# Kernel tuning notes

Hardware: AMD Instinct MI355X
Metric: run time of the kernel (lower is better)

Reference implementation:

```python
import jax, jax.numpy as jnp
import numpy as np

B, H, W = 16, 128, 128
CIN, HID, OUT = 1, 64, 1
WS, NH = 8, 4  # window size, num heads
HD = HID // NH  # head dim = 16


def setup_inputs() -> dict:
    key = jax.random.key(0)
    ks = jax.random.split(key, 32)
    s = 0.05
    d = {"x": jax.random.normal(ks[0], (B, H, W, CIN), jnp.float32)}
    ins = [CIN, HID]
    for l in range(2):
        cin = ins[l]
        kb = 1 + 7 * l
        d[f"conv_w{l}"] = jax.random.normal(ks[kb], (4 * HID, cin + HID, 3, 3), jnp.float32) * s
        d[f"conv_b{l}"] = jnp.zeros((4 * HID,), jnp.float32)
        d[f"px_w{l}"] = jax.random.normal(ks[kb + 1], (HID, cin, 3, 3), jnp.float32) * s
        d[f"py_w{l}"] = jax.random.normal(ks[kb + 2], (HID, cin, 3, 3), jnp.float32) * s
        d[f"qkv_w{l}"] = jax.random.normal(ks[kb + 3], (3 * HID, HID), jnp.float32) * s
        d[f"proj_w{l}"] = jax.random.normal(ks[kb + 4], (HID, HID), jnp.float32) * s
        d[f"proj_b{l}"] = jnp.zeros((HID,), jnp.float32)
    d["out_w"] = jax.random.normal(ks[20], (OUT, HID, 1, 1), jnp.float32) * s
    d["out_b"] = jnp.zeros((OUT,), jnp.float32)
    return d


def _conv(x, w, pad, b=None):
    y = jax.lax.conv_general_dilated(
        x, w, (1, 1), [(pad, pad), (pad, pad)],
        dimension_numbers=("NCHW", "OIHW", "NCHW"))
    if b is not None:
        y = y + b[None, :, None, None]
    return y


def _win_attn(x, qkv_w, proj_w, proj_b):
    # x: [B, H, W, C], H and W are multiples of WS (pad branch is a no-op)
    Bx, Hx, Wx, C = x.shape
    nw_h, nw_w = Hx // WS, Wx // WS
    xw = x.reshape(Bx, nw_h, WS, nw_w, WS, C).transpose(0, 1, 3, 2, 4, 5)
    xw = xw.reshape(-1, WS * WS, C)  # [N, T, C], N = B*nw_h*nw_w, T = 64
    qkv = (xw @ qkv_w.T).reshape(-1, WS * WS, 3, NH, HD).transpose(2, 0, 3, 1, 4)
    q, k, v = qkv[0], qkv[1], qkv[2]  # [N, NH, T, HD]
    attn = jax.nn.softmax(jnp.einsum("nhqd,nhkd->nhqk", q, k) * (HD ** -0.5), axis=-1)
    o = jnp.einsum("nhqk,nhkd->nhqd", attn, v).transpose(0, 2, 1, 3).reshape(-1, WS * WS, C)
    o = o @ proj_w.T + proj_b
    o = o.reshape(Bx, nw_h, nw_w, WS, WS, C).transpose(0, 1, 3, 2, 4, 5)
    return o.reshape(Bx, Hx, Wx, C)


def _cell(x, h, c, cw, cb, pxw, pyw, qw, pw, pb):
    # x: [B, Cin, H, W]; h, c: [B, HID, H, W]
    cc = _conv(jnp.concatenate([x, h], axis=1), cw, 1, cb)
    ci, cf, co, cg = jnp.split(cc, 4, axis=1)
    px = _conv(x, pxw, 1)
    py = _conv(x, pyw, 1)
    i = jax.nn.sigmoid(ci + px)
    f = jax.nn.sigmoid(cf + px)
    o = jax.nn.sigmoid(co + py)
    g = jnp.tanh(cg + py)
    c2 = f * c + i * g
    h2 = o * jnp.tanh(c2)
    h2 = _win_attn(h2.transpose(0, 2, 3, 1), qw, pw, pb).transpose(0, 3, 1, 2)
    return h2, c2


def reference(x, conv_w0, conv_b0, px_w0, py_w0, qkv_w0, proj_w0, proj_b0,
              conv_w1, conv_b1, px_w1, py_w1, qkv_w1, proj_w1, proj_b1,
              out_w, out_b):
    # 4D input path: [B,H,W,C] -> NCHW frame, seq_len = 1
    xin = x.transpose(0, 3, 1, 2)
    z = jnp.zeros((B, HID, H, W), x.dtype)
    h0, _ = _cell(xin, z, z, conv_w0, conv_b0, px_w0, py_w0, qkv_w0, proj_w0, proj_b0)
    h1, _ = _cell(h0, z, z, conv_w1, conv_b1, px_w1, py_w1, qkv_w1, proj_w1, proj_b1)
    out = _conv(h1, out_w, 0, out_b)  # 1x1 output conv on last layer's (T=1) output
    return out.transpose(0, 2, 3, 1)  # [B, H, W, OUT]
```

## Files before the change

kernel.cpp:

```cpp
#include <hip/hip_runtime.h>


#define DEVFN __device__ __forceinline__

typedef __attribute__((ext_vector_type(8))) short short8;
typedef __attribute__((ext_vector_type(4))) float f32x4;

DEVFN float sigmoidf_(float z) { return 1.0f / (1.0f + __expf(-z)); }

DEVFN float tanhf_(float x) {
    float e = __expf(2.0f * x);
    return 1.0f - 2.0f / (e + 1.0f);
}

DEVFN unsigned short f2bf(float f) {
    unsigned int u = __builtin_bit_cast(unsigned int, f);
    u += 0x7fffu + ((u >> 16) & 1u);
    return (unsigned short)(u >> 16);
}

DEVFN unsigned pkbf(float a, float b) {
    return (unsigned)f2bf(a) | ((unsigned)f2bf(b) << 16);
}

__global__ __launch_bounds__(256) void repack_kernel(
    const float* __restrict__ cw0, const float* __restrict__ pxw0, const float* __restrict__ pyw0,
    const float* __restrict__ cw1, const float* __restrict__ pxw1, const float* __restrict__ pyw1,
    const float* __restrict__ qkvw0, const float* __restrict__ projw0,
    const float* __restrict__ qkvw1, const float* __restrict__ projw1,
    unsigned short* __restrict__ pwc, float* __restrict__ pw0,
    unsigned short* __restrict__ qb0, unsigned short* __restrict__ pjb0,
    unsigned short* __restrict__ qb1, unsigned short* __restrict__ pjb1)
{
    int idx = blockIdx.x * 256 + threadIdx.x;
    if (idx < 184320) {
        int j = idx & 7;
        int lane = (idx >> 3) & 63;
        int ng = (idx >> 9) & 3;
        int t = idx >> 11;
        int kk = t % 18, g = t / 18;
        int c = ng * 16 + (lane & 15);
        int kcol = kk * 32 + (lane >> 4) * 8 + j;
        int pos = kcol >> 6, cin = kcol & 63;
        float v;
        if (g == 0)      v = cw1[((c      ) * 128 + cin) * 9 + pos];
        else if (g == 1) v = cw1[((128 + c) * 128 + cin) * 9 + pos];
        else if (g == 2) v = cw1[((192 + c) * 128 + cin) * 9 + pos];
        else if (g == 3) v = pxw1[(c * 64 + cin) * 9 + pos];
        else             v = pyw1[(c * 64 + cin) * 9 + pos];
        pwc[idx] = f2bf(v);
    } else if (idx < 187200) {
        int i2 = idx - 184320;
        int g = i2 / (9 * 64);
        int rem = i2 - g * (9 * 64);
        int pos = rem >> 6, c = rem & 63;
        float v;
        if (g == 0)      v = cw0[(c      ) * 585 + pos];
        else if (g == 1) v = cw0[(128 + c) * 585 + pos];
        else if (g == 2) v = cw0[(192 + c) * 585 + pos];
        else if (g == 3) v = pxw0[c * 9 + pos];
        else             v = pyw0[c * 9 + pos];
        pw0[i2] = v;
    } else if (idx < 187200 + 12288) {
        int i = idx - 187200;           qb0[i] = f2bf(qkvw0[i]);
    } else if (idx < 187200 + 24576) {
        int i = idx - 187200 - 12288;   qb1[i] = f2bf(qkvw1[i]);
    } else if (idx < 187200 + 24576 + 4096) {
        int i = idx - 187200 - 24576;   pjb0[i] = f2bf(projw0[i]);
    } else if (idx < 187200 + 24576 + 8192) {
        int i = idx - 187200 - 28672;   pjb1[i] = f2bf(projw1[i]);
    }
}

__global__ __launch_bounds__(256) void gates1_kernel(
    const float* __restrict__ x, const float* __restrict__ pw,
    const float* __restrict__ cb, unsigned short* __restrict__ dst)
{
    const int idx = blockIdx.x * 256 + threadIdx.x;
    const int pix = idx >> 4, ch0 = (idx & 15) * 4;
    const int b = pix >> 14, y = (pix >> 7) & 127, xq = pix & 127;

    float a[9];
#pragma unroll
    for (int dy = 0; dy < 3; ++dy)
#pragma unroll
        for (int dx = 0; dx < 3; ++dx) {
            int gy = y + dy - 1, gx = xq + dx - 1;
            a[dy * 3 + dx] = ((unsigned)gy < 128u && (unsigned)gx < 128u)
                ? x[(b * 128 + gy) * 128 + gx] : 0.f;
        }

    float acc[5][4];
#pragma unroll
    for (int g = 0; g < 5; ++g)
#pragma unroll
        for (int u = 0; u < 4; ++u) acc[g][u] = 0.f;

#pragma unroll
    for (int pos = 0; pos < 9; ++pos) {
        const float av = a[pos];
#pragma unroll
        for (int g = 0; g < 5; ++g) {
            const float4 w4 = *(const float4*)(pw + (g * 9 + pos) * 64 + ch0);
            acc[g][0] = fmaf(av, w4.x, acc[g][0]);
            acc[g][1] = fmaf(av, w4.y, acc[g][1]);
            acc[g][2] = fmaf(av, w4.z, acc[g][2]);
            acc[g][3] = fmaf(av, w4.w, acc[g][3]);
        }
    }

    float hv[4];
#pragma unroll
    for (int u = 0; u < 4; ++u) {
        float ci = acc[0][u] + cb[ch0 + u];
        float co = acc[1][u] + cb[128 + ch0 + u];
        float cg = acc[2][u] + cb[192 + ch0 + u];
        float iv = sigmoidf_(ci + acc[3][u]);
        float ov = sigmoidf_(co + acc[4][u]);
        float gv = tanhf_(cg + acc[4][u]);
        hv[u] = ov * tanhf_(iv * gv);
    }
    uint2 o;
    o.x = pkbf(hv[0], hv[1]);
    o.y = pkbf(hv[2], hv[3]);
    *(uint2*)(dst + (size_t)pix * 64 + ch0) = o;
}

__global__ __launch_bounds__(256, 3) void gates64_kernel(
    const unsigned short* __restrict__ src, const unsigned short* __restrict__ wtc,
    const float* __restrict__ cb, unsigned short* __restrict__ dst)
{
    __shared__ unsigned short lds[3 * 66 * 64];
    char* const sbase = (char*)lds;

    const int tid = threadIdx.x;
    const int bid = blockIdx.x;
    const int xt = bid & 1, y = (bid >> 1) & 127, b = bid >> 8;
    const int x0 = xt * 64;

    for (int i4 = tid; i4 < 3 * 66 * 8; i4 += 256) {
        int r = i4 / (66 * 8);
        int rem = i4 - r * (66 * 8);
        int xx = rem >> 3, c8 = rem & 7;
        int gy = y + r - 1, gx = x0 + xx - 1;
        uint4 wv = make_uint4(0, 0, 0, 0);
        if ((unsigned)gy < 128u && (unsigned)gx < 128u)
            wv = *(const uint4*)(src + (((size_t)(b * 128 + gy) * 128 + gx) * 64 + c8 * 8));
        int addr = ((r * 66 + xx) * 128 + c8 * 16) ^ ((xx & 7) << 4);
        *(uint4*)(sbase + addr) = wv;
    }
    __syncthreads();

    const int lane = tid & 63;
    const int wv_ = tid >> 6;
    const int r0 = lane & 15;
    const int hi = lane >> 4;
    const int wch = wv_ * 16 + r0;

    const unsigned short* wbase = wtc + (size_t)(wv_ * 64 + lane) * 8;

    f32x4 acc[4][5];
#pragma unroll
    for (int mt = 0; mt < 4; ++mt)
#pragma unroll
        for (int g = 0; g < 5; ++g) acc[mt][g] = (f32x4){0.f, 0.f, 0.f, 0.f};

#pragma unroll
    for (int kk = 0; kk < 18; ++kk) {
        const int pos = kk >> 1, dy = pos / 3, dx = pos % 3, chalf = kk & 1;
        const int swz = (((r0 + dx) & 7) << 4);
        short8 bfr[5];
#pragma unroll
        for (int g = 0; g < 5; ++g)
            bfr[g] = *(const short8*)(wbase + (g * 18 + kk) * 2048);
        short8 afr[4];
#pragma unroll
        for (int mt = 0; mt < 4; ++mt) {
            const int row = dy * 66 + mt * 16 + r0 + dx;
            const int addr = (row * 128 + chalf * 64 + hi * 16) ^ swz;
            afr[mt] = *(const short8*)(sbase + addr);
        }
#pragma unroll
        for (int mt = 0; mt < 4; ++mt)
#pragma unroll
            for (int g = 0; g < 5; ++g)
                acc[mt][g] = __builtin_amdgcn_mfma_f32_16x16x32_bf16(
                    afr[mt], bfr[g], acc[mt][g], 0, 0, 0);
    }

    const float bci = cb[wch], bco = cb[128 + wch], bcg = cb[192 + wch];
    const int rowbase = (b * 128 + y) * 128 + x0;
#pragma unroll
    for (int mt = 0; mt < 4; ++mt) {
#pragma unroll
        for (int rg = 0; rg < 4; ++rg) {
            const int px_i = mt * 16 + hi * 4 + rg;
            float ci = acc[mt][0][rg] + bci;
            float co = acc[mt][1][rg] + bco;
            float cg = acc[mt][2][rg] + bcg;
            float pxv = acc[mt][3][rg];
            float pyv = acc[mt][4][rg];
            float iv = sigmoidf_(ci + pxv);
            float ov = sigmoidf_(co + pyv);
            float gv = tanhf_(cg + pyv);
            dst[(size_t)(rowbase + px_i) * 64 + wch] = f2bf(ov * tanhf_(iv * gv));
        }
    }
}

template <int FUSE>
__global__ __launch_bounds__(256, 3) void attn_kernel(
    const unsigned short* __restrict__ src,
    const unsigned short* __restrict__ qkvwb,
    const unsigned short* __restrict__ projwb,
    const float* __restrict__ projb,
    unsigned short* __restrict__ dst,
    const float* __restrict__ outw,
    const float* __restrict__ outb,
    float* __restrict__ out)
{
    __shared__ char sm[49152];
    char* const Xs = sm;
    char* const Xo = sm + 8192;
    char* const Qa = sm + 16384;
    char* const Ka = sm + 24576;
    char* const VT = sm + 32768;
    char* const Ps = sm + 40960;

    const int tid = threadIdx.x;
    const int lane = tid & 63;
    const int w = __builtin_amdgcn_readfirstlane(tid >> 6);
    const int lo = lane & 15, hi = lane >> 4;
    const int wid = blockIdx.x;
    const int b = wid >> 8, rem = wid & 255, wy = rem >> 4, wx = rem & 15;
    const int pixbase = (b * 128 + wy * 8) * 128 + wx * 8;

    {
        const int t = tid >> 2, c0 = (tid & 3) * 16;
        const int pix = pixbase + (t >> 3) * 128 + (t & 7);
        const uint4* sp = (const uint4*)(src + (size_t)pix * 64 + c0);
        uint4 w0 = sp[0], w1 = sp[1];
        const int a = t * 128 + c0 * 2, sz = (t & 7) << 4;
        *(uint4*)(Xs + (a ^ sz)) = w0;
        *(uint4*)(Xs + ((a + 16) ^ sz)) = w1;
    }
    __syncthreads();

    const int trow = w * 16 + lo;
    const int tswz = (lo & 7) << 4;

#pragma unroll
    for (int h = 0; h < 4; ++h) {
        f32x4 cq = {0.f, 0.f, 0.f, 0.f}, ck = cq, cv = cq;
#pragma unroll
        for (int ks = 0; ks < 2; ++ks) {
            const int koff = hi * 8 + ks * 32;
            short8 xb = *(const short8*)(Xs + ((trow * 128 + koff * 2) ^ tswz));
            short8 aq = *(const short8*)(qkvwb + (h * 16 + lo) * 64 + koff);
            short8 ak = *(const short8*)(qkvwb + (64 + h * 16 + lo) * 64 + koff);
            short8 bv = *(const short8*)(qkvwb + (128 + h * 16 + lo) * 64 + koff);
            cq = __builtin_amdgcn_mfma_f32_16x16x32_bf16(aq, xb, cq, 0, 0, 0);
            ck = __builtin_amdgcn_mfma_f32_16x16x32_bf16(ak, xb, ck, 0, 0, 0);
            cv = __builtin_amdgcn_mfma_f32_16x16x32_bf16(xb, bv, cv, 0, 0, 0);
        }
        uint2 qw, kw, vw;
        qw.x = pkbf(cq[0] * 0.125f, cq[1] * 0.125f);
        qw.y = pkbf(cq[2] * 0.125f, cq[3] * 0.125f);
        kw.x = pkbf(ck[0], ck[1]); kw.y = pkbf(ck[2], ck[3]);
        vw.x = pkbf(cv[0], cv[1]); vw.y = pkbf(cv[2], cv[3]);
        *(uint2*)(Qa + ((trow * 128 + (h * 16 + hi * 4) * 2) ^ tswz)) = qw;
        *(uint2*)(Ka + ((trow * 128 + (h * 16 + hi * 4) * 2) ^ tswz)) = kw;
        *(uint2*)(VT + (((h * 16 + lo) * 128 + (w * 16 + hi * 4) * 2) ^ ((lo & 7) << 4))) = vw;
    }
    __syncthreads();

#pragma unroll 1
    for (int h = 0; h < 4; ++h) {
        const int hb = h * 32;
        short8 bq = *(const short8*)(Qa + ((trow * 128 + hb + (hi & 1) * 16) ^ tswz));
        f32x4 st[4];
#pragma unroll
        for (int mt = 0; mt < 4; ++mt) {
            short8 ak2 = *(const short8*)(Ka + (((mt * 16 + lo) * 128 + hb + (hi & 1) * 16) ^ ((lo & 7) << 4)));
            f32x4 z = {0.f, 0.f, 0.f, 0.f};
            st[mt] = __builtin_amdgcn_mfma_f32_16x16x32_bf16(ak2, bq, z, 0, 0, 0);
        }
        float mx = -1e30f;
#pragma unroll
        for (int mt = 0; mt < 4; ++mt)
#pragma unroll
            for (int r = 0; r < 4; ++r) mx = fmaxf(mx, st[mt][r]);
        mx = fmaxf(mx, __shfl_xor(mx, 16));
        mx = fmaxf(mx, __shfl_xor(mx, 32));
        float pv[16];
        float sum = 0.f;
#pragma unroll
        for (int mt = 0; mt < 4; ++mt)
#pragma unroll
            for (int r = 0; r < 4; ++r) {
                float e = __expf(st[mt][r] - mx);
                pv[mt * 4 + r] = e;
                sum += e;
            }
        sum += __shfl_xor(sum, 16);
        sum += __shfl_xor(sum, 32);
        const float rs = 1.0f / sum;
#pragma unroll
        for (int mt = 0; mt < 4; ++mt) {
            uint2 pw_;
            pw_.x = pkbf(pv[mt * 4 + 0] * rs, pv[mt * 4 + 1] * rs);
            pw_.y = pkbf(pv[mt * 4 + 2] * rs, pv[mt * 4 + 3] * rs);
            *(uint2*)(Ps + ((trow * 128 + (mt * 16 + hi * 4) * 2) ^ tswz)) = pw_;
        }
        f32x4 ot = {0.f, 0.f, 0.f, 0.f};
#pragma unroll
        for (int ks = 0; ks < 2; ++ks) {
            const int ko = (hi * 8 + ks * 32) * 2;
            short8 av = *(const short8*)(VT + (((h * 16 + lo) * 128 + ko) ^ ((lo & 7) << 4)));
            short8 bp = *(const short8*)(Ps + ((trow * 128 + ko) ^ tswz));
            ot = __builtin_amdgcn_mfma_f32_16x16x32_bf16(av, bp, ot, 0, 0, 0);
        }
        uint2 ow_;
        ow_.x = pkbf(ot[0], ot[1]); ow_.y = pkbf(ot[2], ot[3]);
        *(uint2*)(Xo + ((trow * 128 + (h * 16 + hi * 4) * 2) ^ tswz)) = ow_;
    }
    __syncthreads();

    f32x4 cy[4];
#pragma unroll
    for (int mt = 0; mt < 4; ++mt) cy[mt] = (f32x4){0.f, 0.f, 0.f, 0.f};
#pragma unroll
    for (int ks = 0; ks < 2; ++ks) {
        const int koff = hi * 8 + ks * 32;
        short8 bw = *(const short8*)(projwb + (w * 16 + lo) * 64 + koff);
#pragma unroll
        for (int mt = 0; mt < 4; ++mt) {
            short8 ax = *(const short8*)(Xo + (((mt * 16 + lo) * 128 + koff * 2) ^ ((lo & 7) << 4)));
            cy[mt] = __builtin_amdgcn_mfma_f32_16x16x32_bf16(ax, bw, cy[mt], 0, 0, 0);
        }
    }
    const float pb = projb[w * 16 + lo];

    if constexpr (FUSE == 0) {
#pragma unroll
        for (int mt = 0; mt < 4; ++mt) {
#pragma unroll
            for (int r = 0; r < 4; ++r) {
                const int tok = mt * 16 + hi * 4 + r;
                const int pix = pixbase + (tok >> 3) * 128 + (tok & 7);
                dst[(size_t)pix * 64 + w * 16 + lo] = f2bf(cy[mt][r] + pb);
            }
        }
    } else {
        const float owv = outw[w * 16 + lo];
        float* red = (float*)VT;
#pragma unroll
        for (int mt = 0; mt < 4; ++mt) {
#pragma unroll
            for (int r = 0; r < 4; ++r) {
                float s = (cy[mt][r] + pb) * owv;
                s += __shfl_xor(s, 1);
                s += __shfl_xor(s, 2);
                s += __shfl_xor(s, 4);
                s += __shfl_xor(s, 8);
                if (lo == 0) red[(mt * 16 + hi * 4 + r) * 4 + w] = s;
            }
        }
        __syncthreads();
        if (tid < 64) {
            const int tok = tid;
            float4 rv = *(const float4*)(red + tok * 4);
            const int pix = pixbase + (tok >> 3) * 128 + (tok & 7);
            out[pix] = (rv.x + rv.y) + (rv.z + rv.w) + outb[0];
        }
    }
}

extern "C" void kernel_launch(void* const* d_in, const int* in_sizes, int n_in,
                              void* d_out, int out_size, void* d_ws, size_t ws_size,
                              hipStream_t stream)
{
    const float* x      = (const float*)d_in[0];
    const float* cw0    = (const float*)d_in[1];
    const float* cb0    = (const float*)d_in[2];
    const float* pxw0   = (const float*)d_in[3];
    const float* pyw0   = (const float*)d_in[4];
    const float* qkvw0  = (const float*)d_in[5];
    const float* projw0 = (const float*)d_in[6];
    const float* projb0 = (const float*)d_in[7];
    const float* cw1    = (const float*)d_in[8];
    const float* cb1    = (const float*)d_in[9];
    const float* pxw1   = (const float*)d_in[10];
    const float* pyw1   = (const float*)d_in[11];
    const float* qkvw1  = (const float*)d_in[12];
    const float* projw1 = (const float*)d_in[13];
    const float* projb1 = (const float*)d_in[14];
    const float* outw   = (const float*)d_in[15];
    const float* outb   = (const float*)d_in[16];

    const size_t BUF = (size_t)16 * 128 * 128 * 64 * sizeof(float);
    char* ws = (char*)d_ws;
    unsigned short* bufA = (unsigned short*)ws;
    unsigned short* bufB = (unsigned short*)(ws + BUF);
    char* wsx = ws + 2 * BUF;
    unsigned short* pwc  = (unsigned short*)(wsx);
    float* pw0           = (float*)(wsx + 369664);
    unsigned short* qb0  = (unsigned short*)(wsx + 381440);
    unsigned short* pjb0 = (unsigned short*)(wsx + 406016);
    unsigned short* qb1  = (unsigned short*)(wsx + 414208);
    unsigned short* pjb1 = (unsigned short*)(wsx + 438784);

    repack_kernel<<<860, 256, 0, stream>>>(
        cw0, pxw0, pyw0, cw1, pxw1, pyw1,
        qkvw0, projw0, qkvw1, projw1,
        pwc, pw0, qb0, pjb0, qb1, pjb1);

    gates1_kernel<<<16384, 256, 0, stream>>>(x, pw0, cb0, bufA);
    attn_kernel<0><<<4096, 256, 0, stream>>>(bufA, qb0, pjb0, projb0, bufB,
                                             nullptr, nullptr, nullptr);
    gates64_kernel<<<4096, 256, 0, stream>>>(bufB, pwc, cb1, bufA);
    attn_kernel<1><<<4096, 256, 0, stream>>>(bufA, qb1, pjb1, projb1, nullptr,
                                             outw, outb, (float*)d_out);
}
```

Measured before the change: 341.0 us.

## Stage gates1 weights/inputs in LDS, coalesce attn stores, shrink LDS

gates1 now processes one 64-pixel row segment per block. It stages the 5x9x64 weights and the 3x66 input halo in shared memory and loops over 16 channels per thread instead of reloading them from global memory per thread. The first attention kernel writes its projected output to LDS (aliasing the Xs/Ps region), then does coalesced 16-byte stores per pixel rather than scattered 2-byte stores. Attention LDS drops to 40KB to allow more resident blocks, and gates64 launch bounds drop from 3 to 2 waves-per-SIMD minimum. The risks are an extra barrier in attn and lower parallelism in gates1.

```diff
diff --git a/kernel.cpp b/kernel.cpp
--- a/kernel.cpp
+++ b/kernel.cpp
@@ -76,57 +76,72 @@
     const float* __restrict__ x, const float* __restrict__ pw,
     const float* __restrict__ cb, unsigned short* __restrict__ dst)
 {
-    const int idx = blockIdx.x * 256 + threadIdx.x;
-    const int pix = idx >> 4, ch0 = (idx & 15) * 4;
-    const int b = pix >> 14, y = (pix >> 7) & 127, xq = pix & 127;
-
+    __shared__ float wlds[5 * 9 * 64];
+    __shared__ float xp[3 * 66];
+
+    const int tid = threadIdx.x;
+    const int bid = blockIdx.x;
+    const int xt = bid & 1, y = (bid >> 1) & 127, b = bid >> 8;
+    const int x0 = xt * 64;
+
+    for (int i = tid; i < 5 * 9 * 64; i += 256) wlds[i] = pw[i];
+    if (tid < 198) {
+        int r = tid / 66, c = tid - r * 66;
+        int gy = y + r - 1, gx = x0 + c - 1;
+        xp[tid] = ((unsigned)gy < 128u && (unsigned)gx < 128u)
+            ? x[(b * 128 + gy) * 128 + gx] : 0.f;
+    }
+    __syncthreads();
+
+    const int px = tid >> 2, cq = tid & 3;
+    const int ch0 = cq * 16;
     float a[9];
 #pragma unroll
     for (int dy = 0; dy < 3; ++dy)
 #pragma unroll
-        for (int dx = 0; dx < 3; ++dx) {
-            int gy = y + dy - 1, gx = xq + dx - 1;
-            a[dy * 3 + dx] = ((unsigned)gy < 128u && (unsigned)gx < 128u)
-                ? x[(b * 128 + gy) * 128 + gx] : 0.f;
-        }
-
-    float acc[5][4];
-#pragma unroll
-    for (int g = 0; g < 5; ++g)
-#pragma unroll
-        for (int u = 0; u < 4; ++u) acc[g][u] = 0.f;
-
-#pragma unroll
-    for (int pos = 0; pos < 9; ++pos) {
-        const float av = a[pos];
-#pragma unroll
-        for (int g = 0; g < 5; ++g) {
-            const float4 w4 = *(const float4*)(pw + (g * 9 + pos) * 64 + ch0);
-            acc[g][0] = fmaf(av, w4.x, acc[g][0]);
-            acc[g][1] = fmaf(av, w4.y, acc[g][1]);
-            acc[g][2] = fmaf(av, w4.z, acc[g][2]);
-            acc[g][3] = fmaf(av, w4.w, acc[g][3]);
-        }
-    }
-
-    float hv[4];
-#pragma unroll
-    for (int u = 0; u < 4; ++u) {
-        float ci = acc[0][u] + cb[ch0 + u];
-        float co = acc[1][u] + cb[128 + ch0 + u];
-        float cg = acc[2][u] + cb[192 + ch0 + u];
-        float iv = sigmoidf_(ci + acc[3][u]);
-        float ov = sigmoidf_(co + acc[4][u]);
-        float gv = tanhf_(cg + acc[4][u]);
-        hv[u] = ov * tanhf_(iv * gv);
-    }
-    uint2 o;
-    o.x = pkbf(hv[0], hv[1]);
-    o.y = pkbf(hv[2], hv[3]);
-    *(uint2*)(dst + (size_t)pix * 64 + ch0) = o;
-}
-
-__global__ __launch_bounds__(256, 3) void gates64_kernel(
+        for (int dx = 0; dx < 3; ++dx)
+            a[dy * 3 + dx] = xp[dy * 66 + px + dx];
+
+    const size_t obase = (size_t)((b * 128 + y) * 128 + x0 + px) * 64 + ch0;
+#pragma unroll 1
+    for (int u4 = 0; u4 < 4; ++u4) {
+        float acc[5][4];
+#pragma unroll
+        for (int g = 0; g < 5; ++g)
+#pragma unroll
+            for (int u = 0; u < 4; ++u) acc[g][u] = 0.f;
+#pragma unroll
+        for (int pos = 0; pos < 9; ++pos) {
+            const float av = a[pos];
+#pragma unroll
+            for (int g = 0; g < 5; ++g) {
+                const float4 w4 = *(const float4*)(wlds + (g * 9 + pos) * 64 + ch0 + 4 * u4);
+                acc[g][0] = fmaf(av, w4.x, acc[g][0]);
+                acc[g][1] = fmaf(av, w4.y, acc[g][1]);
+                acc[g][2] = fmaf(av, w4.z, acc[g][2]);
+                acc[g][3] = fmaf(av, w4.w, acc[g][3]);
+            }
+        }
+        float hv[4];
+#pragma unroll
+        for (int u = 0; u < 4; ++u) {
+            const int ch = ch0 + 4 * u4 + u;
+            float ci = acc[0][u] + cb[ch];
+            float co = acc[1][u] + cb[128 + ch];
+            float cg = acc[2][u] + cb[192 + ch];
+            float iv = sigmoidf_(ci + acc[3][u]);
+            float ov = sigmoidf_(co + acc[4][u]);
+            float gv = tanhf_(cg + acc[4][u]);
+            hv[u] = ov * tanhf_(iv * gv);
+        }
+        uint2 o;
+        o.x = pkbf(hv[0], hv[1]);
+        o.y = pkbf(hv[2], hv[3]);
+        *(uint2*)(dst + obase + 4 * u4) = o;
+    }
+}
+
+__global__ __launch_bounds__(256, 2) void gates64_kernel(
     const unsigned short* __restrict__ src, const unsigned short* __restrict__ wtc,
     const float* __restrict__ cb, unsigned short* __restrict__ dst)
 {
@@ -219,13 +234,13 @@
     const float* __restrict__ outb,
     float* __restrict__ out)
 {
-    __shared__ char sm[49152];
+    __shared__ char sm[40960];
     char* const Xs = sm;
+    char* const Ps = sm;
     char* const Xo = sm + 8192;
     char* const Qa = sm + 16384;
     char* const Ka = sm + 24576;
     char* const VT = sm + 32768;
-    char* const Ps = sm + 40960;
 
     const int tid = threadIdx.x;
     const int lane = tid & 63;
@@ -342,14 +357,23 @@
     const float pb = projb[w * 16 + lo];
 
     if constexpr (FUSE == 0) {
+        unsigned short* Y = (unsigned short*)Ps;
 #pragma unroll
         for (int mt = 0; mt < 4; ++mt) {
 #pragma unroll
             for (int r = 0; r < 4; ++r) {
                 const int tok = mt * 16 + hi * 4 + r;
-                const int pix = pixbase + (tok >> 3) * 128 + (tok & 7);
-                dst[(size_t)pix * 64 + w * 16 + lo] = f2bf(cy[mt][r] + pb);
+                Y[tok * 64 + w * 16 + lo] = f2bf(cy[mt][r] + pb);
             }
+        }
+        __syncthreads();
+        {
+            const int t = tid >> 2, c0 = (tid & 3) * 16;
+            const int pix = pixbase + (t >> 3) * 128 + (t & 7);
+            const uint4* yp = (const uint4*)(Y + t * 64 + c0);
+            uint4* dp = (uint4*)(dst + (size_t)pix * 64 + c0);
+            dp[0] = yp[0];
+            dp[1] = yp[1];
         }
     } else {
         const float owv = outw[w * 16 + lo];
@@ -415,7 +439,7 @@
         qkvw0, projw0, qkvw1, projw1,
         pwc, pw0, qb0, pjb0, qb1, pjb1);
 
-    gates1_kernel<<<16384, 256, 0, stream>>>(x, pw0, cb0, bufA);
+    gates1_kernel<<<4096, 256, 0, stream>>>(x, pw0, cb0, bufA);
     attn_kernel<0><<<4096, 256, 0, stream>>>(bufA, qb0, pjb0, projb0, bufB,
                                              nullptr, nullptr, nullptr);
     gates64_kernel<<<4096, 256, 0, stream>>>(bufB, pwc, cb1, bufA);
```

After: 290.2 us, median of 2. -14.9%, faster.
